# Kernel optimization log

Measured on AMD Instinct MI355X. Metric: run time of the kernel, lower is better.

The kernel has to match this reference:

```python
import jax, jax.numpy as jnp
import numpy as np

N_NODES = 50000
N_EDGES = 800000
IN_CH = 128
HID = 128
OUT_CH = 16
N_LAYERS = 3
N_GRAPHS = 128
BN_EPS = 1e-5


def setup_inputs() -> dict:
    key = jax.random.key(0)
    ks = jax.random.split(key, 12)
    x = jax.random.normal(ks[0], (N_NODES, IN_CH), dtype=jnp.float32)
    edge_index = jax.random.randint(ks[1], (2, N_EDGES), 0, N_NODES, dtype=jnp.int64)
    batch = jnp.sort(jax.random.randint(ks[2], (N_NODES,), 0, N_GRAPHS, dtype=jnp.int64))
    s = 1.0 / np.sqrt(HID)
    W1 = jax.random.normal(ks[3], (N_LAYERS, IN_CH, HID), dtype=jnp.float32) * s
    b1 = jax.random.normal(ks[4], (N_LAYERS, HID), dtype=jnp.float32) * s
    W2 = jax.random.normal(ks[5], (N_LAYERS, HID, HID), dtype=jnp.float32) * s
    b2 = jax.random.normal(ks[6], (N_LAYERS, HID), dtype=jnp.float32) * s
    gamma = jnp.ones((N_LAYERS, HID), dtype=jnp.float32)
    beta = jnp.zeros((N_LAYERS, HID), dtype=jnp.float32)
    mean = jax.random.normal(ks[7], (N_LAYERS, HID), dtype=jnp.float32) * 0.1
    var = jax.random.uniform(ks[8], (N_LAYERS, HID), dtype=jnp.float32, minval=0.5, maxval=1.5)
    Wc = jax.random.normal(ks[9], (HID, OUT_CH), dtype=jnp.float32) * s
    bc = jax.random.normal(ks[10], (OUT_CH,), dtype=jnp.float32) * s
    return {"x": x, "edge_index": edge_index, "batch": batch, "W1": W1, "b1": b1,
            "W2": W2, "b2": b2, "gamma": gamma, "beta": beta, "mean": mean,
            "var": var, "Wc": Wc, "bc": bc}


def reference(x, edge_index, batch, W1, b1, W2, b2, gamma, beta, mean, var, Wc, bc):
    # GIN (eval mode: BN uses running stats, dropout is identity).
    src, dst = edge_index[0], edge_index[1]
    n = x.shape[0]
    h = x
    for i in range(N_LAYERS):
        # GINConv with eps=0: MLP(x + sum_{j->i} x_j)
        agg = jax.ops.segment_sum(h[src], dst, num_segments=n)  # [N, d]
        z = h + agg
        z = jnp.maximum(z @ W1[i] + b1[i], 0.0) @ W2[i] + b2[i]  # 2-layer MLP
        # BatchNorm1d (eval) + ReLU
        inv = gamma[i] * jax.lax.rsqrt(var[i] + BN_EPS)
        h = jnp.maximum((z - mean[i]) * inv + beta[i], 0.0)
    pooled = jax.ops.segment_sum(h, batch, num_segments=N_GRAPHS)  # [G, hid]
    return pooled @ Wc + bc
```

## Files before the change

kernel.cpp:

```cpp
#include <hip/hip_runtime.h>

#define N_NODES 50000
#define N_EDGES 800000
#define CH 128
#define N_GRAPHS 128
#define N_LAYERS 3
#define OUT_CH 16
#define BN_EPS 1e-5f
#define NSPLIT 16
#define NB 196
#define BCAP 4608
#define EPB 4096
#define NTILES (N_NODES / 16)
#define SSTRIDE 20
#define CB 6250
#define SB 196
#define PB 388

typedef unsigned short ushort_t;
typedef __attribute__((ext_vector_type(8))) short bf16x8;
typedef __attribute__((ext_vector_type(4))) float f32x4;

__device__ inline ushort_t f2b(float f) {
    unsigned u = __float_as_uint(f);
    unsigned r = (u + 0x7fffu + ((u >> 16) & 1u)) >> 16;
    return (ushort_t)r;
}
__device__ inline float b2f(ushort_t b) { return __uint_as_float((unsigned)b << 16); }
__device__ inline float blo(unsigned u) { return __uint_as_float(u << 16); }
__device__ inline float bhi(unsigned u) { return __uint_as_float(u & 0xffff0000u); }

__global__ __launch_bounds__(256) void setup_kernel(
    const float4* __restrict__ x, ushort4* __restrict__ xb, int* __restrict__ gcur,
    const int* __restrict__ batch, int* __restrict__ starts, float* __restrict__ pooled,
    const float* __restrict__ W1, const float* __restrict__ W2, ushort_t* __restrict__ Wt,
    const float* __restrict__ b1, const float* __restrict__ b2,
    const float* __restrict__ gamma, const float* __restrict__ beta,
    const float* __restrict__ mean, const float* __restrict__ var,
    float* __restrict__ scale, float* __restrict__ shift) {
    int bid = blockIdx.x, t = threadIdx.x;
    if (bid < CB) {
        int i = bid * 256 + t;
        if (i < NB) gcur[i] = 0;
        float4 v = x[i];
        ushort4 o;
        o.x = f2b(v.x); o.y = f2b(v.y); o.z = f2b(v.z); o.w = f2b(v.w);
        xb[i] = o;
    } else if (bid < CB + SB) {
        int i = (bid - CB) * 256 + t;
        if (i < N_GRAPHS * CH) pooled[i] = 0.f;
        if (i >= N_NODES) return;
        int b = batch[i];
        if (i == 0) {
            for (int g = 0; g <= b; ++g) starts[g] = 0;
        } else {
            int pb = batch[i - 1];
            for (int g = pb + 1; g <= b; ++g) starts[g] = i;
        }
        if (i == N_NODES - 1) {
            for (int g = b + 1; g <= N_GRAPHS; ++g) starts[g] = N_NODES;
        }
    } else {
        int i = (bid - CB - SB) * 256 + t;
        if (i < 6 * CH * CH) {
            int mat = i >> 14, r = i & 16383;
            int j = r & 7, bb = r >> 3;
            int lane = bb & 63, cs = bb >> 6;
            int ct = cs >> 2, ks = cs & 3;
            int n = ct * 16 + (lane & 15);
            int k = ks * 32 + (lane >> 4) * 8 + j;
            const float* Wsrc = (mat < 3) ? (W1 + (size_t)mat * CH * CH)
                                          : (W2 + (size_t)(mat - 3) * CH * CH);
            Wt[i] = f2b(Wsrc[k * CH + n]);
        } else {
            int e = i - 6 * CH * CH;
            if (e >= 6 * CH) return;
            int mat = e / CH, c = e % CH;
            if (mat < 3) {
                scale[e] = 1.f;
                shift[e] = b1[mat * CH + c];
            } else {
                int l = mat - 3;
                float inv = gamma[l * CH + c] * rsqrtf(var[l * CH + c] + BN_EPS);
                scale[e] = inv;
                shift[e] = (b2[l * CH + c] - mean[l * CH + c]) * inv + beta[l * CH + c];
            }
        }
    }
}

__global__ __launch_bounds__(256) void bin_kernel(const int* __restrict__ src,
                                                  const int* __restrict__ dst,
                                                  int* __restrict__ gcur,
                                                  unsigned* __restrict__ gbuck) {
    __shared__ int lcnt[256];
    __shared__ int lpref[256];
    __shared__ int lpos[NB];
    __shared__ int lbase[NB];
    __shared__ unsigned stage[EPB];
    __shared__ unsigned char sbk[EPB];
    int t = threadIdx.x;
    int e0 = blockIdx.x * EPB;
    int nloc = N_EDGES - e0; if (nloc > EPB) nloc = EPB;

    lcnt[t] = 0;
    __syncthreads();

    int2 ed[16];
    #pragma unroll
    for (int j = 0; j < 16; ++j) {
        int i = j * 256 + t;
        if (i < nloc) {
            ed[j].x = src[e0 + i];
            ed[j].y = dst[e0 + i];
            atomicAdd(&lcnt[ed[j].y >> 8], 1);
        } else ed[j].y = -1;
    }
    __syncthreads();
    int v = lcnt[t];
    lpref[t] = v;
    __syncthreads();
    for (int off = 1; off < 256; off <<= 1) {
        int y = (t >= off) ? lpref[t - off] : 0;
        __syncthreads();
        lpref[t] += y;
        __syncthreads();
    }
    int excl = lpref[t] - v;
    __syncthreads();
    lpref[t] = excl;
    if (t < NB) {
        lpos[t] = excl;
        lbase[t] = atomicAdd(&gcur[t], v);
    }
    __syncthreads();
    #pragma unroll
    for (int j = 0; j < 16; ++j) {
        if (ed[j].y >= 0) {
            int b = ed[j].y >> 8;
            int slot = atomicAdd(&lpos[b], 1);
            stage[slot] = (unsigned)ed[j].x | ((unsigned)(ed[j].y & 255) << 16);
            sbk[slot] = (unsigned char)b;
        }
    }
    __syncthreads();
    for (int i = t; i < nloc; i += 256) {
        int b = sbk[i];
        gbuck[(size_t)b * BCAP + lbase[b] + (i - lpref[b])] = stage[i];
    }
}

__global__ __launch_bounds__(256) void place_kernel(const int* __restrict__ gcur,
                                                    const unsigned* __restrict__ gbuck,
                                                    int* __restrict__ rowptr,
                                                    ushort_t* __restrict__ esrc) {
    __shared__ ushort_t ssrc[BCAP];
    __shared__ unsigned char sd[BCAP];
    __shared__ int outS[BCAP];
    __shared__ int cnt[256], pref[256], cur[256];
    __shared__ int sscan[256];
    int b = blockIdx.x, t = threadIdx.x;
    int gv = (t < NB) ? gcur[t] : 0;
    sscan[t] = gv;
    cnt[t] = 0;
    __syncthreads();
    for (int off = 1; off < 256; off <<= 1) {
        int y = (t >= off) ? sscan[t - off] : 0;
        __syncthreads();
        sscan[t] += y;
        __syncthreads();
    }
    int nb = gcur[b];
    int base = sscan[b] - nb;
    for (int i = t; i < nb; i += 256) {
        unsigned p = gbuck[(size_t)b * BCAP + i];
        ssrc[i] = (ushort_t)(p & 0xffffu);
        int dl = (p >> 16) & 0xff;
        sd[i] = (unsigned char)dl;
        atomicAdd(&cnt[dl], 1);
    }
    __syncthreads();
    int v = cnt[t];
    pref[t] = v;
    __syncthreads();
    for (int off = 1; off < 256; off <<= 1) {
        int y = (t >= off) ? pref[t - off] : 0;
        __syncthreads();
        pref[t] += y;
        __syncthreads();
    }
    int excl = pref[t] - v;
    __syncthreads();
    pref[t] = excl;
    cur[t] = 0;
    int idx = (b << 8) + t;
    if (idx < N_NODES) rowptr[idx] = base + excl;
    if (b == NB - 1 && t == 0) rowptr[N_NODES] = N_EDGES;
    __syncthreads();
    for (int i = t; i < nb; i += 256) {
        int dl = sd[i];
        int p = pref[dl] + atomicAdd(&cur[dl], 1);
        outS[p] = ssrc[i];
    }
    __syncthreads();
    for (int i = t; i < nb; i += 256)
        esrc[base + i] = (ushort_t)outS[i];
}

__global__ __launch_bounds__(256) void agg_kernel(const unsigned* __restrict__ h2,
                                                  const int* __restrict__ rowptr,
                                                  const ushort_t* __restrict__ esrc,
                                                  unsigned* __restrict__ z2) {
    int wid = (blockIdx.x * 256 + threadIdx.x) >> 6;
    int lane = threadIdx.x & 63;
    if (wid >= N_NODES) return;
    unsigned self = h2[(size_t)wid * 64 + lane];
    float ax = blo(self), ay = bhi(self);
    int e = rowptr[wid], end = rowptr[wid + 1];
    for (; e + 16 <= end; e += 16) {
        unsigned u[16];
        #pragma unroll
        for (int j = 0; j < 16; ++j) {
            int s = esrc[e + j];
            u[j] = h2[(size_t)s * 64 + lane];
        }
        #pragma unroll
        for (int j = 0; j < 16; ++j) { ax += blo(u[j]); ay += bhi(u[j]); }
    }
    for (; e + 8 <= end; e += 8) {
        unsigned u[8];
        #pragma unroll
        for (int j = 0; j < 8; ++j) {
            int s = esrc[e + j];
            u[j] = h2[(size_t)s * 64 + lane];
        }
        #pragma unroll
        for (int j = 0; j < 8; ++j) { ax += blo(u[j]); ay += bhi(u[j]); }
    }
    for (; e + 4 <= end; e += 4) {
        unsigned u[4];
        #pragma unroll
        for (int j = 0; j < 4; ++j) {
            int s = esrc[e + j];
            u[j] = h2[(size_t)s * 64 + lane];
        }
        #pragma unroll
        for (int j = 0; j < 4; ++j) { ax += blo(u[j]); ay += bhi(u[j]); }
    }
    for (; e < end; ++e) {
        unsigned u = h2[(size_t)esrc[e] * 64 + lane];
        ax += blo(u); ay += bhi(u);
    }
    z2[(size_t)wid * 64 + lane] = ((unsigned)f2b(ay) << 16) | (unsigned)f2b(ax);
}

__global__ __launch_bounds__(512) void mlp_kernel(const ushort_t* __restrict__ A,
                                                  const ushort_t* __restrict__ Wf1,
                                                  const ushort_t* __restrict__ Wf2,
                                                  const float* __restrict__ shift1,
                                                  const float* __restrict__ scale2,
                                                  const float* __restrict__ shift2,
                                                  ushort_t* __restrict__ Out) {
    __shared__ ushort_t sW1[CH * CH];
    __shared__ ushort_t sW2[CH * CH];
    __shared__ ushort_t sS[8][CH * SSTRIDE];

    int t = threadIdx.x;
    int wave = t >> 6, lane = t & 63;
    int quad = lane >> 4, l16 = lane & 15;

    {
        const uint4* g1 = (const uint4*)Wf1;
        const uint4* g2 = (const uint4*)Wf2;
        uint4* s1 = (uint4*)sW1;
        uint4* s2 = (uint4*)sW2;
        for (int i = t; i < 2048; i += 512) { s1[i] = g1[i]; s2[i] = g2[i]; }
    }
    __syncthreads();

    const bf16x8* w1f = (const bf16x8*)sW1;
    const bf16x8* w2f = (const bf16x8*)sW2;
    int wg = blockIdx.x * 8 + wave;

    for (int it = 0; it < 2; ++it) {
        int tile = wg + 2048 * it;
        if (tile >= NTILES) break;
        int arow = tile * 16 + l16;

        bf16x8 af[4];
        #pragma unroll
        for (int ks = 0; ks < 4; ++ks)
            af[ks] = *(const bf16x8*)(A + (size_t)arow * CH + ks * 32 + quad * 8);

        f32x4 acc[8];
        #pragma unroll
        for (int ct = 0; ct < 8; ++ct) acc[ct] = (f32x4){0.f, 0.f, 0.f, 0.f};
        #pragma unroll
        for (int ct = 0; ct < 8; ++ct)
            #pragma unroll
            for (int ks = 0; ks < 4; ++ks)
                acc[ct] = __builtin_amdgcn_mfma_f32_16x16x32_bf16(
                    af[ks], w1f[(ct * 4 + ks) * 64 + lane], acc[ct], 0, 0, 0);

        #pragma unroll
        for (int ct = 0; ct < 8; ++ct) {
            int k = ct * 16 + l16;
            float sh = shift1[k];
            uint2 p;
            p.x = ((unsigned)f2b(fmaxf(acc[ct][1] + sh, 0.f)) << 16)
                |  (unsigned)f2b(fmaxf(acc[ct][0] + sh, 0.f));
            p.y = ((unsigned)f2b(fmaxf(acc[ct][3] + sh, 0.f)) << 16)
                |  (unsigned)f2b(fmaxf(acc[ct][2] + sh, 0.f));
            *(uint2*)&sS[wave][k * SSTRIDE + quad * 4] = p;
        }

        bf16x8 af2[4];
        #pragma unroll
        for (int ks = 0; ks < 4; ++ks)
            #pragma unroll
            for (int j = 0; j < 8; ++j)
                af2[ks][j] = (short)sS[wave][(ks * 32 + quad * 8 + j) * SSTRIDE + l16];

        f32x4 acc2[8];
        #pragma unroll
        for (int ct = 0; ct < 8; ++ct) acc2[ct] = (f32x4){0.f, 0.f, 0.f, 0.f};
        #pragma unroll
        for (int ct = 0; ct < 8; ++ct)
            #pragma unroll
            for (int ks = 0; ks < 4; ++ks)
                acc2[ct] = __builtin_amdgcn_mfma_f32_16x16x32_bf16(
                    af2[ks], w2f[(ct * 4 + ks) * 64 + lane], acc2[ct], 0, 0, 0);

        int row0 = tile * 16;
        #pragma unroll
        for (int ct = 0; ct < 8; ++ct) {
            int col = ct * 16 + l16;
            float sc = scale2[col], sh = shift2[col];
            #pragma unroll
            for (int r = 0; r < 4; ++r) {
                int row = row0 + quad * 4 + r;
                Out[(size_t)row * CH + col] = f2b(fmaxf(acc2[ct][r] * sc + sh, 0.f));
            }
        }
    }
}

__global__ __launch_bounds__(64) void pool_kernel(const unsigned* __restrict__ h2,
                                                  const int* __restrict__ starts,
                                                  float* __restrict__ pooled) {
    int g = blockIdx.x >> 4, s = blockIdx.x & 15;
    int c = threadIdx.x;
    int beg = starts[g], end = starts[g + 1];
    float s0 = 0.f, s1 = 0.f;
    for (int n = beg + s; n < end; n += NSPLIT) {
        unsigned u = h2[(size_t)n * 64 + c];
        s0 += blo(u); s1 += bhi(u);
    }
    atomicAdd(&pooled[g * CH + 2 * c], s0);
    atomicAdd(&pooled[g * CH + 2 * c + 1], s1);
}

__global__ __launch_bounds__(256) void cls_kernel(const float* __restrict__ pooled,
                                                  const float* __restrict__ Wc,
                                                  const float* __restrict__ bc,
                                                  float* __restrict__ out) {
    int i = blockIdx.x * blockDim.x + threadIdx.x;
    if (i >= N_GRAPHS * OUT_CH) return;
    int g = i / OUT_CH, o = i % OUT_CH;
    float s = bc[o];
    for (int k = 0; k < CH; ++k) s += pooled[g * CH + k] * Wc[k * OUT_CH + o];
    out[i] = s;
}

extern "C" void kernel_launch(void* const* d_in, const int* in_sizes, int n_in,
                              void* d_out, int out_size, void* d_ws, size_t ws_size,
                              hipStream_t stream) {
    const float* x     = (const float*)d_in[0];
    const int*   eidx  = (const int*)d_in[1];
    const int*   batch = (const int*)d_in[2];
    const float* W1    = (const float*)d_in[3];
    const float* b1    = (const float*)d_in[4];
    const float* W2    = (const float*)d_in[5];
    const float* b2    = (const float*)d_in[6];
    const float* gamma = (const float*)d_in[7];
    const float* beta  = (const float*)d_in[8];
    const float* mean  = (const float*)d_in[9];
    const float* var   = (const float*)d_in[10];
    const float* Wc    = (const float*)d_in[11];
    const float* bc    = (const float*)d_in[12];
    float* out = (float*)d_out;

    const int* src = eidx;
    const int* dst = eidx + N_EDGES;

    char* w = (char*)d_ws;
    size_t off = 0;
    auto alloc = [&](size_t bytes) { void* p = w + off; off += (bytes + 255) & ~(size_t)255; return p; };
    int*      gcur   = (int*)alloc(NB * 4);
    unsigned* gbuck  = (unsigned*)alloc((size_t)NB * BCAP * 4);
    int*      rowptr = (int*)alloc((N_NODES + 1) * 4);
    ushort_t* esrc   = (ushort_t*)alloc(N_EDGES * 2);
    int*      starts = (int*)alloc((N_GRAPHS + 1) * 4);
    ushort_t* Bh     = (ushort_t*)alloc((size_t)N_NODES * CH * 2);
    ushort_t* Bz     = (ushort_t*)alloc((size_t)N_NODES * CH * 2);
    ushort_t* Wt     = (ushort_t*)alloc((size_t)6 * CH * CH * 2);
    float*    scale  = (float*)alloc(6 * CH * 4);
    float*    shift  = (float*)alloc(6 * CH * 4);
    float*    pooled = (float*)alloc(N_GRAPHS * CH * 4);
    (void)ws_size; (void)n_in; (void)in_sizes; (void)out_size;

    setup_kernel<<<CB + SB + PB, 256, 0, stream>>>(
        (const float4*)x, (ushort4*)Bh, gcur,
        batch, starts, pooled,
        W1, W2, Wt, b1, b2, gamma, beta, mean, var, scale, shift);
    bin_kernel<<<(N_EDGES + EPB - 1) / EPB, 256, 0, stream>>>(src, dst, gcur, gbuck);
    place_kernel<<<NB, 256, 0, stream>>>(gcur, gbuck, rowptr, esrc);

    const int agg_grid = (N_NODES + 3) / 4;

    for (int i = 0; i < N_LAYERS; ++i) {
        agg_kernel<<<agg_grid, 256, 0, stream>>>((const unsigned*)Bh, rowptr, esrc,
                                                 (unsigned*)Bz);
        mlp_kernel<<<256, 512, 0, stream>>>(Bz,
                                            Wt + (size_t)i * CH * CH,
                                            Wt + (size_t)(3 + i) * CH * CH,
                                            shift + i * CH,
                                            scale + (3 + i) * CH,
                                            shift + (3 + i) * CH,
                                            Bh);
    }

    pool_kernel<<<N_GRAPHS * NSPLIT, 64, 0, stream>>>((const unsigned*)Bh, starts, pooled);
    cls_kernel<<<(N_GRAPHS * OUT_CH + 255) / 256, 256, 0, stream>>>(pooled, Wc, bc, out);
}
```

Before: 271.7 us.

## Split aggregation into channel passes with edge-parallel lanes and shuffle reduction

The aggregation kernel now splits the 128 channels into four passes of 16 words each. Within each wave, four groups of 16 lanes handle different edges in parallel, and the partial sums are combined with cross-lane shuffles. Pass-major block ordering keeps each pass's slice of the feature table small, so it should stay cache-resident and reduce the cost of random gathers. In exchange, each pass re-reads rowptr and the edge indices, and each gather is only 64 bytes, which may hurt memory efficiency. The pooling split is also doubled to add parallelism.

```diff
diff --git a/kernel.cpp b/kernel.cpp
--- a/kernel.cpp
+++ b/kernel.cpp
@@ -7,12 +7,13 @@
 #define N_LAYERS 3
 #define OUT_CH 16
 #define BN_EPS 1e-5f
-#define NSPLIT 16
+#define NSPLIT 32
 #define NB 196
 #define BCAP 4608
 #define EPB 4096
 #define NTILES (N_NODES / 16)
 #define SSTRIDE 20
+#define NPASS 4
 #define CB 6250
 #define SB 196
 #define PB 388
@@ -211,47 +212,50 @@
                                                   const int* __restrict__ rowptr,
                                                   const ushort_t* __restrict__ esrc,
                                                   unsigned* __restrict__ z2) {
-    int wid = (blockIdx.x * 256 + threadIdx.x) >> 6;
     int lane = threadIdx.x & 63;
-    if (wid >= N_NODES) return;
-    unsigned self = h2[(size_t)wid * 64 + lane];
-    float ax = blo(self), ay = bhi(self);
-    int e = rowptr[wid], end = rowptr[wid + 1];
+    int e4 = lane >> 4, l16 = lane & 15;
+    int pass = blockIdx.x / (N_NODES / 4);
+    int node = (blockIdx.x % (N_NODES / 4)) * 4 + (threadIdx.x >> 6);
+    int cofs = pass * 16 + l16;
+    const unsigned* hrow = h2 + cofs;
+    int e = rowptr[node], end = rowptr[node + 1];
+    float ax = 0.f, ay = 0.f;
     for (; e + 16 <= end; e += 16) {
-        unsigned u[16];
-        #pragma unroll
-        for (int j = 0; j < 16; ++j) {
-            int s = esrc[e + j];
-            u[j] = h2[(size_t)s * 64 + lane];
-        }
-        #pragma unroll
-        for (int j = 0; j < 16; ++j) { ax += blo(u[j]); ay += bhi(u[j]); }
+        int s0 = esrc[e + e4];
+        int s1 = esrc[e + 4 + e4];
+        int s2 = esrc[e + 8 + e4];
+        int s3 = esrc[e + 12 + e4];
+        unsigned u0 = hrow[(size_t)s0 * 64];
+        unsigned u1 = hrow[(size_t)s1 * 64];
+        unsigned u2 = hrow[(size_t)s2 * 64];
+        unsigned u3 = hrow[(size_t)s3 * 64];
+        ax += blo(u0) + blo(u1) + blo(u2) + blo(u3);
+        ay += bhi(u0) + bhi(u1) + bhi(u2) + bhi(u3);
     }
     for (; e + 8 <= end; e += 8) {
-        unsigned u[8];
-        #pragma unroll
-        for (int j = 0; j < 8; ++j) {
-            int s = esrc[e + j];
-            u[j] = h2[(size_t)s * 64 + lane];
-        }
-        #pragma unroll
-        for (int j = 0; j < 8; ++j) { ax += blo(u[j]); ay += bhi(u[j]); }
+        int s0 = esrc[e + e4];
+        int s1 = esrc[e + 4 + e4];
+        unsigned u0 = hrow[(size_t)s0 * 64];
+        unsigned u1 = hrow[(size_t)s1 * 64];
+        ax += blo(u0) + blo(u1);
+        ay += bhi(u0) + bhi(u1);
     }
     for (; e + 4 <= end; e += 4) {
-        unsigned u[4];
-        #pragma unroll
-        for (int j = 0; j < 4; ++j) {
-            int s = esrc[e + j];
-            u[j] = h2[(size_t)s * 64 + lane];
-        }
-        #pragma unroll
-        for (int j = 0; j < 4; ++j) { ax += blo(u[j]); ay += bhi(u[j]); }
-    }
-    for (; e < end; ++e) {
-        unsigned u = h2[(size_t)esrc[e] * 64 + lane];
-        ax += blo(u); ay += bhi(u);
-    }
-    z2[(size_t)wid * 64 + lane] = ((unsigned)f2b(ay) << 16) | (unsigned)f2b(ax);
+        unsigned u0 = hrow[(size_t)esrc[e + e4] * 64];
+        ax += blo(u0); ay += bhi(u0);
+    }
+    if (e + e4 < end) {
+        unsigned u0 = hrow[(size_t)esrc[e + e4] * 64];
+        ax += blo(u0); ay += bhi(u0);
+    }
+    ax += __shfl_xor(ax, 16); ay += __shfl_xor(ay, 16);
+    ax += __shfl_xor(ax, 32); ay += __shfl_xor(ay, 32);
+    if (e4 == 0) {
+        unsigned self = hrow[(size_t)node * 64];
+        ax += blo(self); ay += bhi(self);
+        unsigned o = ((unsigned)f2b(ay) << 16) | (unsigned)f2b(ax);
+        __builtin_nontemporal_store(o, &z2[(size_t)node * 64 + cofs]);
+    }
 }
 
 __global__ __launch_bounds__(512) void mlp_kernel(const ushort_t* __restrict__ A,
@@ -348,7 +352,7 @@
 __global__ __launch_bounds__(64) void pool_kernel(const unsigned* __restrict__ h2,
                                                   const int* __restrict__ starts,
                                                   float* __restrict__ pooled) {
-    int g = blockIdx.x >> 4, s = blockIdx.x & 15;
+    int g = blockIdx.x / NSPLIT, s = blockIdx.x % NSPLIT;
     int c = threadIdx.x;
     int beg = starts[g], end = starts[g + 1];
     float s0 = 0.f, s1 = 0.f;
@@ -416,7 +420,7 @@
     bin_kernel<<<(N_EDGES + EPB - 1) / EPB, 256, 0, stream>>>(src, dst, gcur, gbuck);
     place_kernel<<<NB, 256, 0, stream>>>(gcur, gbuck, rowptr, esrc);
 
-    const int agg_grid = (N_NODES + 3) / 4;
+    const int agg_grid = NPASS * (N_NODES / 4);
 
     for (int i = 0; i < N_LAYERS; ++i) {
         agg_kernel<<<agg_grid, 256, 0, stream>>>((const unsigned*)Bh, rowptr, esrc,
```

After: 397.8 us. +46.4%, slower.

## Split aggregation wave across two edges and fuse pooling with classifier

Applied to the files above, without the earlier changes.

The aggregation kernel now has each half-wave handle a different edge, with every lane loading 8 bytes (4 bf16 channels) instead of 4. The two halves are combined with a cross-half shuffle and the result is written with a non-temporal store, which gives wider loads and more independent gathers in flight. Pooling is fused with the classifier: each block multiplies its partial sums by Wc, reduces across the wave, and atomically adds into the output, which is pre-initialised with the bias in setup. This removes one kernel launch and the pooled buffer, at the cost of more atomics and doubled pool split.

```diff
diff --git a/kernel.cpp b/kernel.cpp
--- a/kernel.cpp
+++ b/kernel.cpp
@@ -7,7 +7,7 @@
 #define N_LAYERS 3
 #define OUT_CH 16
 #define BN_EPS 1e-5f
-#define NSPLIT 16
+#define NSPLIT 32
 #define NB 196
 #define BCAP 4608
 #define EPB 4096
@@ -20,19 +20,20 @@
 typedef unsigned short ushort_t;
 typedef __attribute__((ext_vector_type(8))) short bf16x8;
 typedef __attribute__((ext_vector_type(4))) float f32x4;
+typedef __attribute__((ext_vector_type(2))) unsigned u32x2;
 
 __device__ inline ushort_t f2b(float f) {
     unsigned u = __float_as_uint(f);
     unsigned r = (u + 0x7fffu + ((u >> 16) & 1u)) >> 16;
     return (ushort_t)r;
 }
-__device__ inline float b2f(ushort_t b) { return __uint_as_float((unsigned)b << 16); }
 __device__ inline float blo(unsigned u) { return __uint_as_float(u << 16); }
 __device__ inline float bhi(unsigned u) { return __uint_as_float(u & 0xffff0000u); }
 
 __global__ __launch_bounds__(256) void setup_kernel(
     const float4* __restrict__ x, ushort4* __restrict__ xb, int* __restrict__ gcur,
-    const int* __restrict__ batch, int* __restrict__ starts, float* __restrict__ pooled,
+    const int* __restrict__ batch, int* __restrict__ starts, float* __restrict__ outinit,
+    const float* __restrict__ bc,
     const float* __restrict__ W1, const float* __restrict__ W2, ushort_t* __restrict__ Wt,
     const float* __restrict__ b1, const float* __restrict__ b2,
     const float* __restrict__ gamma, const float* __restrict__ beta,
@@ -48,7 +49,7 @@
         xb[i] = o;
     } else if (bid < CB + SB) {
         int i = (bid - CB) * 256 + t;
-        if (i < N_GRAPHS * CH) pooled[i] = 0.f;
+        if (i < N_GRAPHS * OUT_CH) outinit[i] = bc[i & (OUT_CH - 1)];
         if (i >= N_NODES) return;
         int b = batch[i];
         if (i == 0) {
@@ -213,45 +214,61 @@
                                                   unsigned* __restrict__ z2) {
     int wid = (blockIdx.x * 256 + threadIdx.x) >> 6;
     int lane = threadIdx.x & 63;
+    int e2 = lane >> 5;
+    int l32 = lane & 31;
     if (wid >= N_NODES) return;
-    unsigned self = h2[(size_t)wid * 64 + lane];
-    float ax = blo(self), ay = bhi(self);
+    const unsigned* hp = h2 + 2 * l32;
+    float ax = 0.f, ay = 0.f, az = 0.f, aw = 0.f;
     int e = rowptr[wid], end = rowptr[wid + 1];
     for (; e + 16 <= end; e += 16) {
-        unsigned u[16];
-        #pragma unroll
-        for (int j = 0; j < 16; ++j) {
-            int s = esrc[e + j];
-            u[j] = h2[(size_t)s * 64 + lane];
-        }
-        #pragma unroll
-        for (int j = 0; j < 16; ++j) { ax += blo(u[j]); ay += bhi(u[j]); }
+        u32x2 u[8];
+        #pragma unroll
+        for (int j = 0; j < 8; ++j) {
+            int s = esrc[e + 2 * j + e2];
+            u[j] = *(const u32x2*)(hp + (size_t)s * 64);
+        }
+        #pragma unroll
+        for (int j = 0; j < 8; ++j) {
+            ax += blo(u[j][0]); ay += bhi(u[j][0]);
+            az += blo(u[j][1]); aw += bhi(u[j][1]);
+        }
     }
     for (; e + 8 <= end; e += 8) {
-        unsigned u[8];
-        #pragma unroll
-        for (int j = 0; j < 8; ++j) {
-            int s = esrc[e + j];
-            u[j] = h2[(size_t)s * 64 + lane];
-        }
-        #pragma unroll
-        for (int j = 0; j < 8; ++j) { ax += blo(u[j]); ay += bhi(u[j]); }
-    }
-    for (; e + 4 <= end; e += 4) {
-        unsigned u[4];
+        u32x2 u[4];
         #pragma unroll
         for (int j = 0; j < 4; ++j) {
-            int s = esrc[e + j];
-            u[j] = h2[(size_t)s * 64 + lane];
-        }
-        #pragma unroll
-        for (int j = 0; j < 4; ++j) { ax += blo(u[j]); ay += bhi(u[j]); }
-    }
-    for (; e < end; ++e) {
-        unsigned u = h2[(size_t)esrc[e] * 64 + lane];
-        ax += blo(u); ay += bhi(u);
-    }
-    z2[(size_t)wid * 64 + lane] = ((unsigned)f2b(ay) << 16) | (unsigned)f2b(ax);
+            int s = esrc[e + 2 * j + e2];
+            u[j] = *(const u32x2*)(hp + (size_t)s * 64);
+        }
+        #pragma unroll
+        for (int j = 0; j < 4; ++j) {
+            ax += blo(u[j][0]); ay += bhi(u[j][0]);
+            az += blo(u[j][1]); aw += bhi(u[j][1]);
+        }
+    }
+    for (; e + 2 <= end; e += 2) {
+        int s = esrc[e + e2];
+        u32x2 u = *(const u32x2*)(hp + (size_t)s * 64);
+        ax += blo(u[0]); ay += bhi(u[0]);
+        az += blo(u[1]); aw += bhi(u[1]);
+    }
+    if (e + e2 < end) {
+        int s = esrc[e + e2];
+        u32x2 u = *(const u32x2*)(hp + (size_t)s * 64);
+        ax += blo(u[0]); ay += bhi(u[0]);
+        az += blo(u[1]); aw += bhi(u[1]);
+    }
+    ax += __shfl_xor(ax, 32); ay += __shfl_xor(ay, 32);
+    az += __shfl_xor(az, 32); aw += __shfl_xor(aw, 32);
+    if (e2 == 0) {
+        u32x2 self = *(const u32x2*)(hp + (size_t)wid * 64);
+        ax += blo(self[0]); ay += bhi(self[0]);
+        az += blo(self[1]); aw += bhi(self[1]);
+        u32x2 o;
+        o[0] = ((unsigned)f2b(ay) << 16) | (unsigned)f2b(ax);
+        o[1] = ((unsigned)f2b(aw) << 16) | (unsigned)f2b(az);
+        __builtin_nontemporal_store(o, (u32x2*)(z2 + (size_t)wid * 64 + 2 * l32));
+    }
 }
 
 __global__ __launch_bounds__(512) void mlp_kernel(const ushort_t* __restrict__ A,
@@ -347,8 +364,9 @@
 
 __global__ __launch_bounds__(64) void pool_kernel(const unsigned* __restrict__ h2,
                                                   const int* __restrict__ starts,
-                                                  float* __restrict__ pooled) {
-    int g = blockIdx.x >> 4, s = blockIdx.x & 15;
+                                                  const float* __restrict__ Wc,
+                                                  float* __restrict__ out) {
+    int g = blockIdx.x / NSPLIT, s = blockIdx.x % NSPLIT;
     int c = threadIdx.x;
     int beg = starts[g], end = starts[g + 1];
     float s0 = 0.f, s1 = 0.f;
@@ -356,20 +374,24 @@
         unsigned u = h2[(size_t)n * 64 + c];
         s0 += blo(u); s1 += bhi(u);
     }
-    atomicAdd(&pooled[g * CH + 2 * c], s0);
-    atomicAdd(&pooled[g * CH + 2 * c + 1], s1);
-}
-
-__global__ __launch_bounds__(256) void cls_kernel(const float* __restrict__ pooled,
-                                                  const float* __restrict__ Wc,
-                                                  const float* __restrict__ bc,
-                                                  float* __restrict__ out) {
-    int i = blockIdx.x * blockDim.x + threadIdx.x;
-    if (i >= N_GRAPHS * OUT_CH) return;
-    int g = i / OUT_CH, o = i % OUT_CH;
-    float s = bc[o];
-    for (int k = 0; k < CH; ++k) s += pooled[g * CH + k] * Wc[k * OUT_CH + o];
-    out[i] = s;
+    float p[OUT_CH];
+    #pragma unroll
+    for (int o = 0; o < OUT_CH; ++o)
+        p[o] = s0 * Wc[(2 * c) * OUT_CH + o] + s1 * Wc[(2 * c + 1) * OUT_CH + o];
+    #pragma unroll
+    for (int o = 0; o < OUT_CH; ++o) {
+        p[o] += __shfl_xor(p[o], 1);
+        p[o] += __shfl_xor(p[o], 2);
+        p[o] += __shfl_xor(p[o], 4);
+        p[o] += __shfl_xor(p[o], 8);
+        p[o] += __shfl_xor(p[o], 16);
+        p[o] += __shfl_xor(p[o], 32);
+    }
+    if (c == 0) {
+        #pragma unroll
+        for (int o = 0; o < OUT_CH; ++o)
+            atomicAdd(&out[g * OUT_CH + o], p[o]);
+    }
 }
 
 extern "C" void kernel_launch(void* const* d_in, const int* in_sizes, int n_in,
@@ -406,12 +428,11 @@
     ushort_t* Wt     = (ushort_t*)alloc((size_t)6 * CH * CH * 2);
     float*    scale  = (float*)alloc(6 * CH * 4);
     float*    shift  = (float*)alloc(6 * CH * 4);
-    float*    pooled = (float*)alloc(N_GRAPHS * CH * 4);
     (void)ws_size; (void)n_in; (void)in_sizes; (void)out_size;
 
     setup_kernel<<<CB + SB + PB, 256, 0, stream>>>(
         (const float4*)x, (ushort4*)Bh, gcur,
-        batch, starts, pooled,
+        batch, starts, out, bc,
         W1, W2, Wt, b1, b2, gamma, beta, mean, var, scale, shift);
     bin_kernel<<<(N_EDGES + EPB - 1) / EPB, 256, 0, stream>>>(src, dst, gcur, gbuck);
     place_kernel<<<NB, 256, 0, stream>>>(gcur, gbuck, rowptr, esrc);
@@ -430,6 +451,5 @@
                                             Bh);
     }
 
-    pool_kernel<<<N_GRAPHS * NSPLIT, 64, 0, stream>>>((const unsigned*)Bh, starts, pooled);
-    cls_kernel<<<(N_GRAPHS * OUT_CH + 255) / 256, 256, 0, stream>>>(pooled, Wc, bc, out);
-}
+    pool_kernel<<<N_GRAPHS * NSPLIT, 64, 0, stream>>>((const unsigned*)Bh, starts, Wc, out);
+}
```

Measured after the change: 291.5 us. 7.3% more time.

## Split fused MLP into two GEMM launches and fold classifier into pooling

Applied to the files above, without the earlier changes.

The fused two-layer MLP kernel, which held both weight matrices and a staging buffer in shared memory, is replaced by a single-GEMM kernel that runs twice per layer and writes the hidden activation to a new global buffer. This cuts shared memory per block and uses one tile per wave over many blocks, aiming for higher occupancy, at the cost of an extra round trip through global memory and one more launch per layer. The separate classifier kernel is removed: the pooling kernel multiplies its partial sums by Wc, reduces across the wave with shuffles and atomically adds into an output pre-initialised with the bias, and the pooling split is doubled. The first GEMM now reads a scale array for the first linear layer, which must be set to ones in setup for correctness.

```diff
diff --git a/kernel.cpp b/kernel.cpp
--- a/kernel.cpp
+++ b/kernel.cpp
@@ -7,12 +7,11 @@
 #define N_LAYERS 3
 #define OUT_CH 16
 #define BN_EPS 1e-5f
-#define NSPLIT 16
+#define NSPLIT 32
 #define NB 196
 #define BCAP 4608
 #define EPB 4096
 #define NTILES (N_NODES / 16)
-#define SSTRIDE 20
 #define CB 6250
 #define SB 196
 #define PB 388
@@ -26,13 +25,13 @@
     unsigned r = (u + 0x7fffu + ((u >> 16) & 1u)) >> 16;
     return (ushort_t)r;
 }
-__device__ inline float b2f(ushort_t b) { return __uint_as_float((unsigned)b << 16); }
 __device__ inline float blo(unsigned u) { return __uint_as_float(u << 16); }
 __device__ inline float bhi(unsigned u) { return __uint_as_float(u & 0xffff0000u); }
 
 __global__ __launch_bounds__(256) void setup_kernel(
     const float4* __restrict__ x, ushort4* __restrict__ xb, int* __restrict__ gcur,
-    const int* __restrict__ batch, int* __restrict__ starts, float* __restrict__ pooled,
+    const int* __restrict__ batch, int* __restrict__ starts, float* __restrict__ outinit,
+    const float* __restrict__ bc,
     const float* __restrict__ W1, const float* __restrict__ W2, ushort_t* __restrict__ Wt,
     const float* __restrict__ b1, const float* __restrict__ b2,
     const float* __restrict__ gamma, const float* __restrict__ beta,
@@ -48,7 +47,7 @@
         xb[i] = o;
     } else if (bid < CB + SB) {
         int i = (bid - CB) * 256 + t;
-        if (i < N_GRAPHS * CH) pooled[i] = 0.f;
+        if (i < N_GRAPHS * OUT_CH) outinit[i] = bc[i & (OUT_CH - 1)];
         if (i >= N_NODES) return;
         int b = batch[i];
         if (i == 0) {
@@ -254,101 +253,59 @@
     z2[(size_t)wid * 64 + lane] = ((unsigned)f2b(ay) << 16) | (unsigned)f2b(ax);
 }
 
-__global__ __launch_bounds__(512) void mlp_kernel(const ushort_t* __restrict__ A,
-                                                  const ushort_t* __restrict__ Wf1,
-                                                  const ushort_t* __restrict__ Wf2,
-                                                  const float* __restrict__ shift1,
-                                                  const float* __restrict__ scale2,
-                                                  const float* __restrict__ shift2,
-                                                  ushort_t* __restrict__ Out) {
-    __shared__ ushort_t sW1[CH * CH];
-    __shared__ ushort_t sW2[CH * CH];
-    __shared__ ushort_t sS[8][CH * SSTRIDE];
-
+__global__ __launch_bounds__(256) void gemm_kernel(const ushort_t* __restrict__ A,
+                                                   const ushort_t* __restrict__ Wf,
+                                                   const float* __restrict__ scale,
+                                                   const float* __restrict__ shift,
+                                                   ushort_t* __restrict__ Out) {
+    __shared__ ushort_t sW[CH * CH];
     int t = threadIdx.x;
     int wave = t >> 6, lane = t & 63;
     int quad = lane >> 4, l16 = lane & 15;
-
     {
-        const uint4* g1 = (const uint4*)Wf1;
-        const uint4* g2 = (const uint4*)Wf2;
-        uint4* s1 = (uint4*)sW1;
-        uint4* s2 = (uint4*)sW2;
-        for (int i = t; i < 2048; i += 512) { s1[i] = g1[i]; s2[i] = g2[i]; }
-    }
-    __syncthreads();
-
-    const bf16x8* w1f = (const bf16x8*)sW1;
-    const bf16x8* w2f = (const bf16x8*)sW2;
-    int wg = blockIdx.x * 8 + wave;
-
-    for (int it = 0; it < 2; ++it) {
-        int tile = wg + 2048 * it;
-        if (tile >= NTILES) break;
-        int arow = tile * 16 + l16;
-
-        bf16x8 af[4];
+        const uint4* g = (const uint4*)Wf;
+        uint4* s = (uint4*)sW;
+        #pragma unroll
+        for (int i = 0; i < 8; ++i) s[i * 256 + t] = g[i * 256 + t];
+    }
+    __syncthreads();
+    const bf16x8* wf = (const bf16x8*)sW;
+
+    int tile = blockIdx.x * 4 + wave;
+    if (tile >= NTILES) return;
+    int arow = tile * 16 + l16;
+
+    bf16x8 af[4];
+    #pragma unroll
+    for (int ks = 0; ks < 4; ++ks)
+        af[ks] = *(const bf16x8*)(A + (size_t)arow * CH + ks * 32 + quad * 8);
+
+    f32x4 acc[8];
+    #pragma unroll
+    for (int ct = 0; ct < 8; ++ct) acc[ct] = (f32x4){0.f, 0.f, 0.f, 0.f};
+    #pragma unroll
+    for (int ct = 0; ct < 8; ++ct)
         #pragma unroll
         for (int ks = 0; ks < 4; ++ks)
-            af[ks] = *(const bf16x8*)(A + (size_t)arow * CH + ks * 32 + quad * 8);
-
-        f32x4 acc[8];
-        #pragma unroll
-        for (int ct = 0; ct < 8; ++ct) acc[ct] = (f32x4){0.f, 0.f, 0.f, 0.f};
-        #pragma unroll
-        for (int ct = 0; ct < 8; ++ct)
-            #pragma unroll
-            for (int ks = 0; ks < 4; ++ks)
-                acc[ct] = __builtin_amdgcn_mfma_f32_16x16x32_bf16(
-                    af[ks], w1f[(ct * 4 + ks) * 64 + lane], acc[ct], 0, 0, 0);
-
-        #pragma unroll
-        for (int ct = 0; ct < 8; ++ct) {
-            int k = ct * 16 + l16;
-            float sh = shift1[k];
-            uint2 p;
-            p.x = ((unsigned)f2b(fmaxf(acc[ct][1] + sh, 0.f)) << 16)
-                |  (unsigned)f2b(fmaxf(acc[ct][0] + sh, 0.f));
-            p.y = ((unsigned)f2b(fmaxf(acc[ct][3] + sh, 0.f)) << 16)
-                |  (unsigned)f2b(fmaxf(acc[ct][2] + sh, 0.f));
-            *(uint2*)&sS[wave][k * SSTRIDE + quad * 4] = p;
-        }
-
-        bf16x8 af2[4];
-        #pragma unroll
-        for (int ks = 0; ks < 4; ++ks)
-            #pragma unroll
-            for (int j = 0; j < 8; ++j)
-                af2[ks][j] = (short)sS[wave][(ks * 32 + quad * 8 + j) * SSTRIDE + l16];
-
-        f32x4 acc2[8];
-        #pragma unroll
-        for (int ct = 0; ct < 8; ++ct) acc2[ct] = (f32x4){0.f, 0.f, 0.f, 0.f};
-        #pragma unroll
-        for (int ct = 0; ct < 8; ++ct)
-            #pragma unroll
-            for (int ks = 0; ks < 4; ++ks)
-                acc2[ct] = __builtin_amdgcn_mfma_f32_16x16x32_bf16(
-                    af2[ks], w2f[(ct * 4 + ks) * 64 + lane], acc2[ct], 0, 0, 0);
-
-        int row0 = tile * 16;
-        #pragma unroll
-        for (int ct = 0; ct < 8; ++ct) {
-            int col = ct * 16 + l16;
-            float sc = scale2[col], sh = shift2[col];
-            #pragma unroll
-            for (int r = 0; r < 4; ++r) {
-                int row = row0 + quad * 4 + r;
-                Out[(size_t)row * CH + col] = f2b(fmaxf(acc2[ct][r] * sc + sh, 0.f));
-            }
-        }
+            acc[ct] = __builtin_amdgcn_mfma_f32_16x16x32_bf16(
+                af[ks], wf[(ct * 4 + ks) * 64 + lane], acc[ct], 0, 0, 0);
+
+    int row0 = tile * 16 + quad * 4;
+    #pragma unroll
+    for (int ct = 0; ct < 8; ++ct) {
+        int col = ct * 16 + l16;
+        float sc = scale[col], sh = shift[col];
+        #pragma unroll
+        for (int r = 0; r < 4; ++r)
+            Out[(size_t)(row0 + r) * CH + col] = f2b(fmaxf(acc[ct][r] * sc + sh, 0.f));
     }
 }
 
 __global__ __launch_bounds__(64) void pool_kernel(const unsigned* __restrict__ h2,
                                                   const int* __restrict__ starts,
-                                                  float* __restrict__ pooled) {
-    int g = blockIdx.x >> 4, s = blockIdx.x & 15;
+                                                  const float* __restrict__ Wc,
+                                                  float* __restrict__ out) {
+    int g = blockIdx.x / NSPLIT, s = blockIdx.x % NSPLIT;
     int c = threadIdx.x;
     int beg = starts[g], end = starts[g + 1];
     float s0 = 0.f, s1 = 0.f;
@@ -356,20 +313,24 @@
         unsigned u = h2[(size_t)n * 64 + c];
         s0 += blo(u); s1 += bhi(u);
     }
-    atomicAdd(&pooled[g * CH + 2 * c], s0);
-    atomicAdd(&pooled[g * CH + 2 * c + 1], s1);
-}
-
-__global__ __launch_bounds__(256) void cls_kernel(const float* __restrict__ pooled,
-                                                  const float* __restrict__ Wc,
-                                                  const float* __restrict__ bc,
-                                                  float* __restrict__ out) {
-    int i = blockIdx.x * blockDim.x + threadIdx.x;
-    if (i >= N_GRAPHS * OUT_CH) return;
-    int g = i / OUT_CH, o = i % OUT_CH;
-    float s = bc[o];
-    for (int k = 0; k < CH; ++k) s += pooled[g * CH + k] * Wc[k * OUT_CH + o];
-    out[i] = s;
+    float p[OUT_CH];
+    #pragma unroll
+    for (int o = 0; o < OUT_CH; ++o)
+        p[o] = s0 * Wc[(2 * c) * OUT_CH + o] + s1 * Wc[(2 * c + 1) * OUT_CH + o];
+    #pragma unroll
+    for (int o = 0; o < OUT_CH; ++o) {
+        p[o] += __shfl_xor(p[o], 1);
+        p[o] += __shfl_xor(p[o], 2);
+        p[o] += __shfl_xor(p[o], 4);
+        p[o] += __shfl_xor(p[o], 8);
+        p[o] += __shfl_xor(p[o], 16);
+        p[o] += __shfl_xor(p[o], 32);
+    }
+    if (c == 0) {
+        #pragma unroll
+        for (int o = 0; o < OUT_CH; ++o)
+            atomicAdd(&out[g * OUT_CH + o], p[o]);
+    }
 }
 
 extern "C" void kernel_launch(void* const* d_in, const int* in_sizes, int n_in,
@@ -403,33 +364,36 @@
     int*      starts = (int*)alloc((N_GRAPHS + 1) * 4);
     ushort_t* Bh     = (ushort_t*)alloc((size_t)N_NODES * CH * 2);
     ushort_t* Bz     = (ushort_t*)alloc((size_t)N_NODES * CH * 2);
+    ushort_t* Bm     = (ushort_t*)alloc((size_t)N_NODES * CH * 2);
     ushort_t* Wt     = (ushort_t*)alloc((size_t)6 * CH * CH * 2);
     float*    scale  = (float*)alloc(6 * CH * 4);
     float*    shift  = (float*)alloc(6 * CH * 4);
-    float*    pooled = (float*)alloc(N_GRAPHS * CH * 4);
     (void)ws_size; (void)n_in; (void)in_sizes; (void)out_size;
 
     setup_kernel<<<CB + SB + PB, 256, 0, stream>>>(
         (const float4*)x, (ushort4*)Bh, gcur,
-        batch, starts, pooled,
+        batch, starts, out, bc,
         W1, W2, Wt, b1, b2, gamma, beta, mean, var, scale, shift);
     bin_kernel<<<(N_EDGES + EPB - 1) / EPB, 256, 0, stream>>>(src, dst, gcur, gbuck);
     place_kernel<<<NB, 256, 0, stream>>>(gcur, gbuck, rowptr, esrc);
 
     const int agg_grid = (N_NODES + 3) / 4;
+    const int gemm_grid = (NTILES + 3) / 4;
 
     for (int i = 0; i < N_LAYERS; ++i) {
         agg_kernel<<<agg_grid, 256, 0, stream>>>((const unsigned*)Bh, rowptr, esrc,
                                                  (unsigned*)Bz);
-        mlp_kernel<<<256, 512, 0, stream>>>(Bz,
-                                            Wt + (size_t)i * CH * CH,
-                                            Wt + (size_t)(3 + i) * CH * CH,
-                                            shift + i * CH,
-                                            scale + (3 + i) * CH,
-                                            shift + (3 + i) * CH,
-                                            Bh);
-    }
-
-    pool_kernel<<<N_GRAPHS * NSPLIT, 64, 0, stream>>>((const unsigned*)Bh, starts, pooled);
-    cls_kernel<<<(N_GRAPHS * OUT_CH + 255) / 256, 256, 0, stream>>>(pooled, Wc, bc, out);
-}
+        gemm_kernel<<<gemm_grid, 256, 0, stream>>>(Bz,
+                                                   Wt + (size_t)i * CH * CH,
+                                                   scale + i * CH,
+                                                   shift + i * CH,
+                                                   Bm);
+        gemm_kernel<<<gemm_grid, 256, 0, stream>>>(Bm,
+                                                   Wt + (size_t)(3 + i) * CH * CH,
+                                                   scale + (3 + i) * CH,
+                                                   shift + (3 + i) * CH,
+                                                   Bh);
+    }
+
+    pool_kernel<<<N_GRAPHS * NSPLIT, 64, 0, stream>>>((const unsigned*)Bh, starts, Wc, out);
+}
```

Measured after the change: 287.7 us. 5.9% more time.
